# Kernel tuning notes

Hardware: AMD Instinct MI355X
Metric: run time of the kernel (lower is better)

Reference implementation:

```python
import jax, jax.numpy as jnp
import numpy as np

N_NODES = 100000
N_EDGES = 1200000
N_GRAPHS = 512
N_REL = 3
NUM_SHAPES = 16
NUM_COLORS = 16
NUM_CLASS = 10


def setup_inputs() -> dict:
    key = jax.random.key(0)
    ks = jax.random.split(key, 16)
    inp = {
        "x": jax.random.randint(ks[0], (N_NODES, 2), 0, NUM_SHAPES),
        "edge_index": jax.random.randint(ks[1], (2, N_EDGES), 0, N_NODES),
        "edge_type": jax.random.randint(ks[2], (N_EDGES,), 0, N_REL),
        "batch": jnp.sort(jax.random.randint(ks[3], (N_NODES,), 0, N_GRAPHS)),
        # parameters
        "se": jax.random.normal(ks[4], (NUM_SHAPES, 8), jnp.float32) * 0.1,
        "ce": jax.random.normal(ks[5], (NUM_COLORS, 8), jnp.float32) * 0.1,
        "pre_w": jax.random.normal(ks[6], (16, 32), jnp.float32) * 0.1,
        "pre_b": jnp.zeros((32,), jnp.float32),
        "w1": jax.random.normal(ks[7], (N_REL, 32, 64), jnp.float32) * 0.1,
        "root1": jax.random.normal(ks[8], (32, 64), jnp.float32) * 0.1,
        "b1": jnp.zeros((64,), jnp.float32),
        "w2": jax.random.normal(ks[9], (N_REL, 64, 64), jnp.float32) * 0.1,
        "root2": jax.random.normal(ks[10], (64, 64), jnp.float32) * 0.1,
        "b2": jnp.zeros((64,), jnp.float32),
        "cls_w": jax.random.normal(ks[11], (64, NUM_CLASS), jnp.float32) * 0.1,
        "cls_b": jnp.zeros((NUM_CLASS,), jnp.float32),
    }
    return inp


def _rgcn(h, src, dst, edge_type, weight, root, bias):
    # PyG RGCNConv with aggr='mean': out = x @ root + bias + sum_r mean_{edges of rel r}(x_j @ W_r)
    out = h @ root + bias
    for r in range(N_REL):
        mask = (edge_type == r)
        hr = h @ weight[r]                      # [N, out] transform-then-gather
        msg = jnp.where(mask[:, None], hr[src], 0.0)  # [E, out]
        agg = jax.ops.segment_sum(msg, dst, num_segments=N_NODES)
        cnt = jax.ops.segment_sum(mask.astype(h.dtype), dst, num_segments=N_NODES)
        out = out + agg / jnp.maximum(cnt, 1.0)[:, None]
    return out


def reference(x, edge_index, edge_type, batch, se, ce, pre_w, pre_b,
              w1, root1, b1, w2, root2, b2, cls_w, cls_b):
    h = jnp.concatenate([se[x[:, 0]], ce[x[:, 1]]], axis=1)  # [N,16]
    h = jax.nn.relu(h @ pre_w + pre_b)                        # [N,32]
    src, dst = edge_index[0], edge_index[1]
    h = jax.nn.relu(_rgcn(h, src, dst, edge_type, w1, root1, b1))  # [N,64]
    h = jax.nn.relu(_rgcn(h, src, dst, edge_type, w2, root2, b2))  # [N,64]
    # global mean pool over graph ids
    s = jax.ops.segment_sum(h, batch, num_segments=N_GRAPHS)
    c = jax.ops.segment_sum(jnp.ones((h.shape[0],), h.dtype), batch, num_segments=N_GRAPHS)
    g = s / jnp.maximum(c, 1.0)[:, None]                      # [G,64]
    return g @ cls_w + cls_b                                  # [G,num_class]
```

## Files before the change

kernel.cpp:

```cpp
#include <hip/hip_runtime.h>

#define NN 100000
#define NE 1200000
#define NG 512
#define NSEG (3 * NN)
#define NC 4
#define CHUNK 1024
#define NCHUNK ((NSEG + CHUNK - 1) / CHUNK)

typedef __bf16 bf16x8 __attribute__((ext_vector_type(8)));
typedef float f32x4 __attribute__((ext_vector_type(4)));

static constexpr size_t AGG_OFF   = 0;
static constexpr size_t AGG_BYTES = (size_t)NSEG * 32 * 4;
static constexpr size_t HIST_OFF  = AGG_OFF + AGG_BYTES;
static constexpr size_t START_OFF = HIST_OFF + (size_t)NC * NSEG * 4;
static constexpr size_t END_OFF   = START_OFF + (size_t)NSEG * 4;
static constexpr size_t COFF_OFF  = END_OFF + (size_t)NSEG * 4;
static constexpr size_t CSUM_OFF  = COFF_OFF + (size_t)NSEG * 4;
static constexpr size_t ESRC_OFF  = CSUM_OFF + 4096;
static constexpr size_t H1_OFF    = ESRC_OFF + (size_t)NE * 4;
static constexpr size_t H2_OFF    = H1_OFF + (size_t)NN * 64 * 2;
static constexpr size_t WT1H_OFF  = H2_OFF + (size_t)NN * 64 * 4;
static constexpr size_t WT1L_OFF  = WT1H_OFF + 64 * 128 * 2;
static constexpr size_t WT2H_OFF  = WT1L_OFF + 64 * 128 * 2;
static constexpr size_t WT2L_OFF  = WT2H_OFF + 64 * 256 * 2;
static constexpr size_t TAB_OFF   = WT2L_OFF + 64 * 256 * 2;
static constexpr size_t CB_OFF    = TAB_OFF + 256 * 32 * 4;
static constexpr size_t RS_OFF    = ((CB_OFF + NN + 15) / 16) * 16;

__device__ __forceinline__ void async_copy16(void* lds, const void* g) {
    __builtin_amdgcn_global_load_lds(
        (const __attribute__((address_space(1))) void*)g,
        (__attribute__((address_space(3))) void*)lds, 16, 0, 0);
}

__device__ __forceinline__ void prepw_elem(const float* root, const float* w,
                                           __bf16* wh, __bf16* wl, int cin, int t) {
    int kt = 4 * cin;
    if (t >= 64 * kt) return;
    int j = t / kt, k = t % kt;
    int sidx = k / cin, kk = k % cin;
    float v = (sidx == 0) ? root[kk * 64 + j]
                          : w[((size_t)(sidx - 1) * cin + kk) * 64 + j];
    __bf16 h = (__bf16)v;
    wh[t] = h;
    wl[t] = (__bf16)(v - (float)h);
}

#define RB_BASE 488
__global__ __launch_bounds__(256)
void k_rank_prep(const int* __restrict__ ei, const int* __restrict__ et,
                 int* __restrict__ hist4, unsigned long long* __restrict__ rs8,
                 const int* __restrict__ x, const float* __restrict__ se,
                 const float* __restrict__ ce, const float* __restrict__ pw,
                 const float* __restrict__ pb,
                 const float* __restrict__ root1, const float* __restrict__ w1,
                 const float* __restrict__ root2, const float* __restrict__ w2,
                 __bf16* __restrict__ wh1, __bf16* __restrict__ wl1,
                 __bf16* __restrict__ wh2, __bf16* __restrict__ wl2,
                 float* __restrict__ table, unsigned char* __restrict__ cb) {
    int b = blockIdx.x, t = threadIdx.x;
    if (b >= RB_BASE) {
        int e = (b - RB_BASE) * 256 + t;
        if (e >= NE) return;
        int s = ei[e];
        int d = ei[NE + e];
        int r = et[e];
        int x0 = x[2 * s], x1 = x[2 * s + 1];
        int seg = r * NN + d;
        int c = e & (NC - 1);
        unsigned int rank = (unsigned int)atomicAdd(&hist4[c * NSEG + seg], 1);
        unsigned int hi = (rank << 19) | (unsigned int)seg;
        unsigned int lo = (unsigned int)(s | ((x0 * 16 + x1) << 17));
        rs8[e] = ((unsigned long long)hi << 32) | lo;
        return;
    }
    if (b < 32) {
        prepw_elem(root1, w1, wh1, wl1, 32, b * 256 + t);
    } else if (b < 96) {
        prepw_elem(root2, w2, wh2, wl2, 64, (b - 32) * 256 + t);
    } else if (b == 96) {
        __shared__ float sW[16 * 32];
        __shared__ float sB[32];
        for (int i = t; i < 512; i += 256) sW[i] = pw[i];
        if (t < 32) sB[t] = pb[t];
        __syncthreads();
        int cmb = t, s = cmb >> 4, c = cmb & 15;
        float in[16];
#pragma unroll
        for (int k = 0; k < 8; k++) in[k] = se[s * 8 + k];
#pragma unroll
        for (int k = 0; k < 8; k++) in[8 + k] = ce[c * 8 + k];
        float acc[32];
#pragma unroll
        for (int j = 0; j < 32; j++) acc[j] = sB[j];
#pragma unroll
        for (int k = 0; k < 16; k++) {
            float hv = in[k];
#pragma unroll
            for (int j = 0; j < 32; j++) acc[j] += hv * sW[k * 32 + j];
        }
        float* o = table + (size_t)cmb * 32;
#pragma unroll
        for (int j = 0; j < 32; j += 4)
            *(float4*)(o + j) = make_float4(fmaxf(acc[j], 0.f), fmaxf(acc[j + 1], 0.f),
                                            fmaxf(acc[j + 2], 0.f), fmaxf(acc[j + 3], 0.f));
    } else {
        int n = (b - 97) * 256 + t;
        if (n < NN) cb[n] = (unsigned char)(x[2 * n] * 16 + x[2 * n + 1]);
    }
}

__global__ __launch_bounds__(256)
void k_chunksum(const int* __restrict__ hist4, int* __restrict__ csum) {
    __shared__ int s[256];
    int b = blockIdx.x, t = threadIdx.x;
    int base = b * CHUNK + t * 4;
    int sum = 0;
#pragma unroll
    for (int k = 0; k < 4; k++) {
        int i = base + k;
        if (i < NSEG) {
#pragma unroll
            for (int c = 0; c < NC; c++) sum += hist4[c * NSEG + i];
        }
    }
    s[t] = sum;
    __syncthreads();
    for (int off = 128; off > 0; off >>= 1) {
        if (t < off) s[t] += s[t + off];
        __syncthreads();
    }
    if (t == 0) csum[b] = s[0];
}

__global__ __launch_bounds__(512)
void k_chunkscan(int* __restrict__ csum) {
    __shared__ int s[512];
    int t = threadIdx.x;
    int v = (t < NCHUNK) ? csum[t] : 0;
    s[t] = v;
    __syncthreads();
    for (int off = 1; off < 512; off <<= 1) {
        int x = (t >= off) ? s[t - off] : 0;
        __syncthreads();
        s[t] += x;
        __syncthreads();
    }
    if (t < NCHUNK) csum[t] = s[t] - v;
}

__global__ __launch_bounds__(256)
void k_localscan(const int* __restrict__ hist4, const int* __restrict__ csum,
                 int* __restrict__ start, int* __restrict__ end, int* __restrict__ coff) {
    __shared__ int s[256];
    int b = blockIdx.x, t = threadIdx.x;
    int base = b * CHUNK + t * 4;
    int tot[4], cofv[4];
    int s4 = 0;
#pragma unroll
    for (int k = 0; k < 4; k++) {
        int i = base + k;
        int c0 = 0, c1 = 0, c2 = 0, c3 = 0;
        if (i < NSEG) {
            c0 = hist4[0 * NSEG + i];
            c1 = hist4[1 * NSEG + i];
            c2 = hist4[2 * NSEG + i];
            c3 = hist4[3 * NSEG + i];
        }
        tot[k] = c0 + c1 + c2 + c3;
        cofv[k] = c0 | ((c0 + c1) << 8) | ((c0 + c1 + c2) << 16);
        s4 += tot[k];
    }
    s[t] = s4;
    __syncthreads();
    for (int off = 1; off < 256; off <<= 1) {
        int x = (t >= off) ? s[t - off] : 0;
        __syncthreads();
        s[t] += x;
        __syncthreads();
    }
    int excl = s[t] - s4 + csum[b];
#pragma unroll
    for (int k = 0; k < 4; k++) {
        int i = base + k;
        if (i < NSEG) {
            start[i] = excl;
            end[i] = excl + tot[k];
            coff[i] = cofv[k];
        }
        excl += tot[k];
    }
}

__global__ __launch_bounds__(256)
void k_fill2(const unsigned long long* __restrict__ rs8,
             const int* __restrict__ start, const int* __restrict__ coff,
             int* __restrict__ esrc) {
    int e = blockIdx.x * 256 + threadIdx.x;
    if (e >= NE) return;
    unsigned long long v = rs8[e];
    unsigned int hi = (unsigned int)(v >> 32);
    int seg = (int)(hi & 0x7FFFFu);
    int rank = (int)(hi >> 19);
    int c = e & (NC - 1);
    int off = c ? ((coff[seg] >> (8 * (c - 1))) & 0xFF) : 0;
    esrc[start[seg] + off + rank] = (int)(unsigned int)v;
}

__global__ __launch_bounds__(256)
void k_gather_t(const int* __restrict__ start, const int* __restrict__ end,
                const int* __restrict__ esrc, const float* __restrict__ table,
                float* __restrict__ agg) {
    int tid = blockIdx.x * 256 + threadIdx.x;
    int seg = tid >> 3;
    int p = tid & 7;
    if (seg >= NSEG) return;
    int st = start[seg], en = end[seg];
    float4 acc = make_float4(0.f, 0.f, 0.f, 0.f);
    int i = st;
    for (; i + 4 <= en; i += 4) {
        int v0 = esrc[i], v1 = esrc[i + 1], v2 = esrc[i + 2], v3 = esrc[i + 3];
        float4 a = *(const float4*)(table + ((v0 >> 17) & 0xFF) * 32 + p * 4);
        float4 b = *(const float4*)(table + ((v1 >> 17) & 0xFF) * 32 + p * 4);
        float4 c = *(const float4*)(table + ((v2 >> 17) & 0xFF) * 32 + p * 4);
        float4 d = *(const float4*)(table + ((v3 >> 17) & 0xFF) * 32 + p * 4);
        acc.x += (a.x + b.x) + (c.x + d.x);
        acc.y += (a.y + b.y) + (c.y + d.y);
        acc.z += (a.z + b.z) + (c.z + d.z);
        acc.w += (a.w + b.w) + (c.w + d.w);
    }
    for (; i < en; i++) {
        int v = esrc[i];
        float4 a = *(const float4*)(table + ((v >> 17) & 0xFF) * 32 + p * 4);
        acc.x += a.x; acc.y += a.y; acc.z += a.z; acc.w += a.w;
    }
    int c = en - st;
    float inv = 1.f / (float)(c > 1 ? c : 1);
    acc.x *= inv; acc.y *= inv; acc.z *= inv; acc.w *= inv;
    *(float4*)(agg + (size_t)seg * 32 + p * 4) = acc;
}

__global__ __launch_bounds__(256)
void k_gather64(const int* __restrict__ start, const int* __restrict__ end,
                const int* __restrict__ esrc, const __bf16* __restrict__ h,
                __bf16* __restrict__ agg) {
    int tid = blockIdx.x * 256 + threadIdx.x;
    int seg = tid >> 3;
    int p = tid & 7;
    if (seg >= NSEG) return;
    int st = start[seg], en = end[seg];
    float acc[8];
#pragma unroll
    for (int j = 0; j < 8; j++) acc[j] = 0.f;
    int i = st;
    for (; i + 4 <= en; i += 4) {
        int s0 = esrc[i] & 0x1FFFF, s1 = esrc[i + 1] & 0x1FFFF;
        int s2 = esrc[i + 2] & 0x1FFFF, s3 = esrc[i + 3] & 0x1FFFF;
        bf16x8 v0 = *(const bf16x8*)(h + (size_t)s0 * 64 + p * 8);
        bf16x8 v1 = *(const bf16x8*)(h + (size_t)s1 * 64 + p * 8);
        bf16x8 v2 = *(const bf16x8*)(h + (size_t)s2 * 64 + p * 8);
        bf16x8 v3 = *(const bf16x8*)(h + (size_t)s3 * 64 + p * 8);
#pragma unroll
        for (int j = 0; j < 8; j++)
            acc[j] += ((float)v0[j] + (float)v1[j]) + ((float)v2[j] + (float)v3[j]);
    }
    for (; i < en; i++) {
        int s = esrc[i] & 0x1FFFF;
        bf16x8 v = *(const bf16x8*)(h + (size_t)s * 64 + p * 8);
#pragma unroll
        for (int j = 0; j < 8; j++) acc[j] += (float)v[j];
    }
    int c = en - st;
    float inv = 1.f / (float)(c > 1 ? c : 1);
    bf16x8 o;
#pragma unroll
    for (int j = 0; j < 8; j++) o[j] = (__bf16)(acc[j] * inv);
    *(bf16x8*)(agg + (size_t)seg * 64 + p * 8) = o;
}

__device__ __forceinline__ void split8(float4 a0, float4 a1, bf16x8& hi, bf16x8& lo) {
    float v[8] = {a0.x, a0.y, a0.z, a0.w, a1.x, a1.y, a1.z, a1.w};
#pragma unroll
    for (int i = 0; i < 8; i++) {
        __bf16 h = (__bf16)v[i];
        hi[i] = h;
        lo[i] = (__bf16)(v[i] - (float)h);
    }
}

__global__ __launch_bounds__(256, 1)
void k_combine_l1(const float* __restrict__ table, const unsigned char* __restrict__ cb,
                  const float* __restrict__ agg,
                  const __bf16* __restrict__ wh, const __bf16* __restrict__ wl,
                  const float* __restrict__ bias, __bf16* __restrict__ h_out) {
    constexpr int KT = 128;
    __shared__ float sIN[64 * 64];
    __shared__ __bf16 sWH[64 * 64];
    __shared__ __bf16 sWL[64 * 64];

    const int tid = threadIdx.x;
    const int wave = tid >> 6;
    const int lane = tid & 63;
    const int cA = lane & 15;
    const int kg = lane >> 4;
    const int n0 = blockIdx.x * 64;

    f32x4 acc[4];
#pragma unroll
    for (int nb = 0; nb < 4; nb++) {
        float bv = bias[nb * 16 + cA];
        acc[nb][0] = bv; acc[nb][1] = bv; acc[nb][2] = bv; acc[nb][3] = bv;
    }

    for (int c = 0; c < 2; c++) {
        if (c) __syncthreads();
#pragma unroll
        for (int i = 0; i < 4; i++) {
            int F = tid + i * 256;
            int row = F >> 4, j = F & 15;
            int jor = j ^ (row & 7);
            int n = n0 + row; if (n > NN - 1) n = NN - 1;
            int sidx = 2 * c + (jor >> 3);
            int jj = jor & 7;
            const float* src = (sidx == 0)
                ? table + (size_t)cb[n] * 32 + jj * 4
                : agg + ((size_t)(sidx - 1) * NN + n) * 32 + jj * 4;
            async_copy16(sIN + (size_t)F * 4, src);
        }
#pragma unroll
        for (int i = 0; i < 2; i++) {
            int F = tid + i * 256;
            int col = F >> 3, s = F & 7;
            int sor = s ^ (col & 7);
            async_copy16(sWH + (size_t)F * 8, wh + (size_t)col * KT + c * 64 + sor * 8);
            async_copy16(sWL + (size_t)F * 8, wl + (size_t)col * KT + c * 64 + sor * 8);
        }
        __syncthreads();
#pragma unroll
        for (int ks = 0; ks < 2; ks++) {
            const int rowL = wave * 16 + cA;
            const int jA = ks * 8 + kg * 2;
            float4 a0 = ((const float4*)sIN)[rowL * 16 + (jA ^ (rowL & 7))];
            float4 a1 = ((const float4*)sIN)[rowL * 16 + ((jA + 1) ^ (rowL & 7))];
            bf16x8 ah, al;
            split8(a0, a1, ah, al);
            const int k8 = ks * 4 + kg;
#pragma unroll
            for (int nb = 0; nb < 4; nb++) {
                const int col = nb * 16 + cA;
                const int bs = col * 8 + (k8 ^ (col & 7));
                bf16x8 bh = ((const bf16x8*)sWH)[bs];
                bf16x8 bl = ((const bf16x8*)sWL)[bs];
                acc[nb] = __builtin_amdgcn_mfma_f32_16x16x32_bf16(ah, bh, acc[nb], 0, 0, 0);
                acc[nb] = __builtin_amdgcn_mfma_f32_16x16x32_bf16(al, bh, acc[nb], 0, 0, 0);
                acc[nb] = __builtin_amdgcn_mfma_f32_16x16x32_bf16(ah, bl, acc[nb], 0, 0, 0);
                acc[nb] = __builtin_amdgcn_mfma_f32_16x16x32_bf16(al, bl, acc[nb], 0, 0, 0);
            }
        }
    }
#pragma unroll
    for (int nb = 0; nb < 4; nb++) {
#pragma unroll
        for (int r = 0; r < 4; r++) {
            int n = n0 + wave * 16 + kg * 4 + r;
            if (n < NN)
                h_out[(size_t)n * 64 + nb * 16 + cA] = (__bf16)fmaxf(acc[nb][r], 0.f);
        }
    }
}

__global__ __launch_bounds__(256, 1)
void k_combine_l2(const __bf16* __restrict__ h1b, const __bf16* __restrict__ aggb,
                  const __bf16* __restrict__ wh, const __bf16* __restrict__ wl,
                  const float* __restrict__ bias, float* __restrict__ h_out) {
    constexpr int KT = 256;
    __shared__ __bf16 sINb[64 * 64];
    __shared__ __bf16 sWH[64 * 64];
    __shared__ __bf16 sWL[64 * 64];

    const int tid = threadIdx.x;
    const int wave = tid >> 6;
    const int lane = tid & 63;
    const int cA = lane & 15;
    const int kg = lane >> 4;
    const int n0 = blockIdx.x * 64;

    f32x4 acc[4];
#pragma unroll
    for (int nb = 0; nb < 4; nb++) {
        float bv = bias[nb * 16 + cA];
        acc[nb][0] = bv; acc[nb][1] = bv; acc[nb][2] = bv; acc[nb][3] = bv;
    }

    for (int c = 0; c < 4; c++) {
        if (c) __syncthreads();
#pragma unroll
        for (int i = 0; i < 2; i++) {
            int F = tid + i * 256;
            int row = F >> 3, j = F & 7;
            int jor = j ^ (row & 7);
            int n = n0 + row; if (n > NN - 1) n = NN - 1;
            const __bf16* src = (c == 0)
                ? h1b + (size_t)n * 64 + jor * 8
                : aggb + ((size_t)(c - 1) * NN + n) * 64 + jor * 8;
            async_copy16(sINb + (size_t)F * 8, src);
        }
#pragma unroll
        for (int i = 0; i < 2; i++) {
            int F = tid + i * 256;
            int col = F >> 3, s = F & 7;
            int sor = s ^ (col & 7);
            async_copy16(sWH + (size_t)F * 8, wh + (size_t)col * KT + c * 64 + sor * 8);
            async_copy16(sWL + (size_t)F * 8, wl + (size_t)col * KT + c * 64 + sor * 8);
        }
        __syncthreads();
#pragma unroll
        for (int ks = 0; ks < 2; ks++) {
            const int rowL = wave * 16 + cA;
            const int s8 = ks * 4 + kg;
            bf16x8 ah = ((const bf16x8*)sINb)[rowL * 8 + (s8 ^ (rowL & 7))];
#pragma unroll
            for (int nb = 0; nb < 4; nb++) {
                const int col = nb * 16 + cA;
                const int bs = col * 8 + (s8 ^ (col & 7));
                bf16x8 bh = ((const bf16x8*)sWH)[bs];
                bf16x8 bl = ((const bf16x8*)sWL)[bs];
                acc[nb] = __builtin_amdgcn_mfma_f32_16x16x32_bf16(ah, bh, acc[nb], 0, 0, 0);
                acc[nb] = __builtin_amdgcn_mfma_f32_16x16x32_bf16(ah, bl, acc[nb], 0, 0, 0);
            }
        }
    }
#pragma unroll
    for (int nb = 0; nb < 4; nb++) {
#pragma unroll
        for (int r = 0; r < 4; r++) {
            int n = n0 + wave * 16 + kg * 4 + r;
            if (n < NN)
                h_out[(size_t)n * 64 + nb * 16 + cA] = fmaxf(acc[nb][r], 0.f);
        }
    }
}

__global__ __launch_bounds__(256)
void k_pool_final(const float* __restrict__ h, const int* __restrict__ batch,
                  const float* __restrict__ cw, const float* __restrict__ cbias,
                  float* __restrict__ out) {
    int g = blockIdx.x;
    auto lb = [&](int v) {
        int lo = 0, hi = NN;
        while (lo < hi) {
            int m = (lo + hi) >> 1;
            if (batch[m] < v) lo = m + 1; else hi = m;
        }
        return lo;
    };
    int st = lb(g), en = lb(g + 1);
    int col = threadIdx.x & 63, chunk = threadIdx.x >> 6;
    float acc = 0.f;
    for (int n = st + chunk; n < en; n += 4) acc += h[(size_t)n * 64 + col];
    __shared__ float s[256];
    __shared__ float mean[64];
    s[threadIdx.x] = acc;
    __syncthreads();
    if (chunk == 0) {
        float tot = s[col] + s[64 + col] + s[128 + col] + s[192 + col];
        int c = en - st;
        mean[col] = tot / (float)(c > 1 ? c : 1);
    }
    __syncthreads();
    if (threadIdx.x < 10) {
        int j = threadIdx.x;
        float o = cbias[j];
#pragma unroll
        for (int k = 0; k < 64; k++) o += mean[k] * cw[k * 10 + j];
        out[g * 10 + j] = o;
    }
}

extern "C" void kernel_launch(void* const* d_in, const int* in_sizes, int n_in,
                              void* d_out, int out_size, void* d_ws, size_t ws_size,
                              hipStream_t stream) {
    const int* x      = (const int*)d_in[0];
    const int* ei     = (const int*)d_in[1];
    const int* et     = (const int*)d_in[2];
    const int* batch  = (const int*)d_in[3];
    const float* se   = (const float*)d_in[4];
    const float* ce   = (const float*)d_in[5];
    const float* pw   = (const float*)d_in[6];
    const float* pb   = (const float*)d_in[7];
    const float* w1   = (const float*)d_in[8];
    const float* root1= (const float*)d_in[9];
    const float* b1   = (const float*)d_in[10];
    const float* w2   = (const float*)d_in[11];
    const float* root2= (const float*)d_in[12];
    const float* b2   = (const float*)d_in[13];
    const float* cw   = (const float*)d_in[14];
    const float* cbias= (const float*)d_in[15];
    float* out = (float*)d_out;

    char* ws = (char*)d_ws;
    float*  agg1 = (float*)(ws + AGG_OFF);
    __bf16* aggb = (__bf16*)(ws + AGG_OFF);
    int*   hist4 = (int*)(ws + HIST_OFF);
    int*   start = (int*)(ws + START_OFF);
    int*   end   = (int*)(ws + END_OFF);
    int*   coff  = (int*)(ws + COFF_OFF);
    int*   csum  = (int*)(ws + CSUM_OFF);
    int*   esrc  = (int*)(ws + ESRC_OFF);
    __bf16* h1b  = (__bf16*)(ws + H1_OFF);
    float* h2    = (float*)(ws + H2_OFF);
    __bf16* wt1h = (__bf16*)(ws + WT1H_OFF);
    __bf16* wt1l = (__bf16*)(ws + WT1L_OFF);
    __bf16* wt2h = (__bf16*)(ws + WT2H_OFF);
    __bf16* wt2l = (__bf16*)(ws + WT2L_OFF);
    float* table = (float*)(ws + TAB_OFF);
    unsigned char* cbarr = (unsigned char*)(ws + CB_OFF);
    unsigned long long* rs8 = (unsigned long long*)(ws + RS_OFF);

    (void)hipMemsetAsync(hist4, 0, (size_t)NC * NSEG * 4, stream);

    int rank_blocks = RB_BASE + (NE + 255) / 256;
    k_rank_prep<<<rank_blocks, 256, 0, stream>>>(ei, et, hist4, rs8,
                                                 x, se, ce, pw, pb, root1, w1, root2, w2,
                                                 wt1h, wt1l, wt2h, wt2l, table, cbarr);

    k_chunksum<<<NCHUNK, 256, 0, stream>>>(hist4, csum);
    k_chunkscan<<<1, 512, 0, stream>>>(csum);
    k_localscan<<<NCHUNK, 256, 0, stream>>>(hist4, csum, start, end, coff);
    k_fill2<<<(NE + 255) / 256, 256, 0, stream>>>(rs8, start, coff, esrc);

    k_gather_t<<<(NSEG * 8 + 255) / 256, 256, 0, stream>>>(start, end, esrc, table, agg1);
    k_combine_l1<<<(NN + 63) / 64, 256, 0, stream>>>(table, cbarr, agg1,
                                                     wt1h, wt1l, b1, h1b);
    k_gather64<<<(NSEG * 8 + 255) / 256, 256, 0, stream>>>(start, end, esrc, h1b, aggb);
    k_combine_l2<<<(NN + 63) / 64, 256, 0, stream>>>(h1b, aggb,
                                                     wt2h, wt2l, b2, h2);

    k_pool_final<<<NG, 256, 0, stream>>>(h2, batch, cw, cbias, out);
}
```

Baseline: 197.4 us.

## Precompute layer-1 transformed combo tables and fuse gather with combine

Each node's layer-1 input depends only on its 256 possible (shape,color) combos, so the code now precomputes the combo table multiplied by root1 (plus bias) and by each relation weight, giving four 256x64 tables. A single kernel then gathers the transformed rows per relation, mean-normalises, adds the root term, applies ReLU and writes h1 in bf16. This removes the float agg1 intermediate and the MFMA combine_l1 kernel. In exchange, gathered rows are twice as wide (64 floats instead of 32) and one thread loops over all three relations serially.

```diff
diff --git a/kernel.cpp b/kernel.cpp
--- a/kernel.cpp
+++ b/kernel.cpp
@@ -12,7 +12,7 @@
 typedef float f32x4 __attribute__((ext_vector_type(4)));
 
 static constexpr size_t AGG_OFF   = 0;
-static constexpr size_t AGG_BYTES = (size_t)NSEG * 32 * 4;
+static constexpr size_t AGG_BYTES = (size_t)NSEG * 64 * 2;
 static constexpr size_t HIST_OFF  = AGG_OFF + AGG_BYTES;
 static constexpr size_t START_OFF = HIST_OFF + (size_t)NC * NSEG * 4;
 static constexpr size_t END_OFF   = START_OFF + (size_t)NSEG * 4;
@@ -21,12 +21,10 @@
 static constexpr size_t ESRC_OFF  = CSUM_OFF + 4096;
 static constexpr size_t H1_OFF    = ESRC_OFF + (size_t)NE * 4;
 static constexpr size_t H2_OFF    = H1_OFF + (size_t)NN * 64 * 2;
-static constexpr size_t WT1H_OFF  = H2_OFF + (size_t)NN * 64 * 4;
-static constexpr size_t WT1L_OFF  = WT1H_OFF + 64 * 128 * 2;
-static constexpr size_t WT2H_OFF  = WT1L_OFF + 64 * 128 * 2;
+static constexpr size_t WT2H_OFF  = H2_OFF + (size_t)NN * 64 * 4;
 static constexpr size_t WT2L_OFF  = WT2H_OFF + 64 * 256 * 2;
-static constexpr size_t TAB_OFF   = WT2L_OFF + 64 * 256 * 2;
-static constexpr size_t CB_OFF    = TAB_OFF + 256 * 32 * 4;
+static constexpr size_t TW_OFF    = WT2L_OFF + 64 * 256 * 2;
+static constexpr size_t CB_OFF    = TW_OFF + 4 * 256 * 64 * 4;
 static constexpr size_t RS_OFF    = ((CB_OFF + NN + 15) / 16) * 16;
 
 __device__ __forceinline__ void async_copy16(void* lds, const void* g) {
@@ -48,7 +46,28 @@
     wl[t] = (__bf16)(v - (float)h);
 }
 
-#define RB_BASE 488
+__device__ __forceinline__ void combo_row(int cmb, const float* se, const float* ce,
+                                          const float* sW, const float* sB, float* outr) {
+    int s = cmb >> 4, c = cmb & 15;
+    float in[16];
+#pragma unroll
+    for (int k = 0; k < 8; k++) in[k] = se[s * 8 + k];
+#pragma unroll
+    for (int k = 0; k < 8; k++) in[8 + k] = ce[c * 8 + k];
+    float acc[32];
+#pragma unroll
+    for (int j = 0; j < 32; j++) acc[j] = sB[j];
+#pragma unroll
+    for (int k = 0; k < 16; k++) {
+        float hv = in[k];
+#pragma unroll
+        for (int j = 0; j < 32; j++) acc[j] += hv * sW[k * 32 + j];
+    }
+#pragma unroll
+    for (int j = 0; j < 32; j++) outr[j] = fmaxf(acc[j], 0.f);
+}
+
+#define RB_BASE 471
 __global__ __launch_bounds__(256)
 void k_rank_prep(const int* __restrict__ ei, const int* __restrict__ et,
                  int* __restrict__ hist4, unsigned long long* __restrict__ rs8,
@@ -56,10 +75,10 @@
                  const float* __restrict__ ce, const float* __restrict__ pw,
                  const float* __restrict__ pb,
                  const float* __restrict__ root1, const float* __restrict__ w1,
+                 const float* __restrict__ b1,
                  const float* __restrict__ root2, const float* __restrict__ w2,
-                 __bf16* __restrict__ wh1, __bf16* __restrict__ wl1,
                  __bf16* __restrict__ wh2, __bf16* __restrict__ wl2,
-                 float* __restrict__ table, unsigned char* __restrict__ cb) {
+                 float* __restrict__ tw, unsigned char* __restrict__ cb) {
     int b = blockIdx.x, t = threadIdx.x;
     if (b >= RB_BASE) {
         int e = (b - RB_BASE) * 256 + t;
@@ -76,38 +95,40 @@
         rs8[e] = ((unsigned long long)hi << 32) | lo;
         return;
     }
-    if (b < 32) {
-        prepw_elem(root1, w1, wh1, wl1, 32, b * 256 + t);
-    } else if (b < 96) {
-        prepw_elem(root2, w2, wh2, wl2, 64, (b - 32) * 256 + t);
-    } else if (b == 96) {
+    if (b < 64) {
+        prepw_elem(root2, w2, wh2, wl2, 64, b * 256 + t);
+    } else if (b < 80) {
         __shared__ float sW[16 * 32];
         __shared__ float sB[32];
+        __shared__ float sTab[256 * 33];
         for (int i = t; i < 512; i += 256) sW[i] = pw[i];
         if (t < 32) sB[t] = pb[t];
         __syncthreads();
-        int cmb = t, s = cmb >> 4, c = cmb & 15;
-        float in[16];
-#pragma unroll
-        for (int k = 0; k < 8; k++) in[k] = se[s * 8 + k];
-#pragma unroll
-        for (int k = 0; k < 8; k++) in[8 + k] = ce[c * 8 + k];
-        float acc[32];
-#pragma unroll
-        for (int j = 0; j < 32; j++) acc[j] = sB[j];
-#pragma unroll
-        for (int k = 0; k < 16; k++) {
-            float hv = in[k];
-#pragma unroll
-            for (int j = 0; j < 32; j++) acc[j] += hv * sW[k * 32 + j];
-        }
-        float* o = table + (size_t)cmb * 32;
-#pragma unroll
-        for (int j = 0; j < 32; j += 4)
-            *(float4*)(o + j) = make_float4(fmaxf(acc[j], 0.f), fmaxf(acc[j + 1], 0.f),
-                                            fmaxf(acc[j + 2], 0.f), fmaxf(acc[j + 3], 0.f));
+        {
+            float row[32];
+            combo_row(t, se, ce, sW, sB, row);
+#pragma unroll
+            for (int j = 0; j < 32; j++) sTab[t * 33 + j] = row[j];
+        }
+        __syncthreads();
+        int ti = (b - 64) >> 2;
+        int row = ((b - 64) & 3) * 64 + (t >> 2);
+        int c0 = (t & 3) * 16;
+        const float* Wsrc = (ti == 0) ? root1 : (w1 + (size_t)(ti - 1) * 32 * 64);
+        float acc[16];
+#pragma unroll
+        for (int j = 0; j < 16; j++) acc[j] = (ti == 0) ? b1[c0 + j] : 0.f;
+        for (int k = 0; k < 32; k++) {
+            float hv = sTab[row * 33 + k];
+#pragma unroll
+            for (int j = 0; j < 16; j++) acc[j] += hv * Wsrc[k * 64 + c0 + j];
+        }
+        float* o = tw + (size_t)ti * 256 * 64 + (size_t)row * 64 + c0;
+#pragma unroll
+        for (int j = 0; j < 16; j += 4)
+            *(float4*)(o + j) = make_float4(acc[j], acc[j + 1], acc[j + 2], acc[j + 3]);
     } else {
-        int n = (b - 97) * 256 + t;
+        int n = (b - 80) * 256 + t;
         if (n < NN) cb[n] = (unsigned char)(x[2 * n] * 16 + x[2 * n + 1]);
     }
 }
@@ -210,36 +231,42 @@
 }
 
 __global__ __launch_bounds__(256)
-void k_gather_t(const int* __restrict__ start, const int* __restrict__ end,
-                const int* __restrict__ esrc, const float* __restrict__ table,
-                float* __restrict__ agg) {
+void k_l1(const int* __restrict__ start, const int* __restrict__ end,
+          const int* __restrict__ esrc, const unsigned char* __restrict__ cb,
+          const float* __restrict__ tw, __bf16* __restrict__ h1b) {
     int tid = blockIdx.x * 256 + threadIdx.x;
-    int seg = tid >> 3;
+    int n = tid >> 3;
     int p = tid & 7;
-    if (seg >= NSEG) return;
-    int st = start[seg], en = end[seg];
-    float4 acc = make_float4(0.f, 0.f, 0.f, 0.f);
-    int i = st;
-    for (; i + 4 <= en; i += 4) {
-        int v0 = esrc[i], v1 = esrc[i + 1], v2 = esrc[i + 2], v3 = esrc[i + 3];
-        float4 a = *(const float4*)(table + ((v0 >> 17) & 0xFF) * 32 + p * 4);
-        float4 b = *(const float4*)(table + ((v1 >> 17) & 0xFF) * 32 + p * 4);
-        float4 c = *(const float4*)(table + ((v2 >> 17) & 0xFF) * 32 + p * 4);
-        float4 d = *(const float4*)(table + ((v3 >> 17) & 0xFF) * 32 + p * 4);
-        acc.x += (a.x + b.x) + (c.x + d.x);
-        acc.y += (a.y + b.y) + (c.y + d.y);
-        acc.z += (a.z + b.z) + (c.z + d.z);
-        acc.w += (a.w + b.w) + (c.w + d.w);
-    }
-    for (; i < en; i++) {
-        int v = esrc[i];
-        float4 a = *(const float4*)(table + ((v >> 17) & 0xFF) * 32 + p * 4);
-        acc.x += a.x; acc.y += a.y; acc.z += a.z; acc.w += a.w;
-    }
-    int c = en - st;
-    float inv = 1.f / (float)(c > 1 ? c : 1);
-    acc.x *= inv; acc.y *= inv; acc.z *= inv; acc.w *= inv;
-    *(float4*)(agg + (size_t)seg * 32 + p * 4) = acc;
+    if (n >= NN) return;
+    const float* tr = tw + (size_t)cb[n] * 64 + p * 8;
+    float4 a0 = *(const float4*)tr;
+    float4 a1 = *(const float4*)(tr + 4);
+#pragma unroll
+    for (int r = 0; r < 3; r++) {
+        const float* tb = tw + (size_t)(r + 1) * 256 * 64 + p * 8;
+        int seg = r * NN + n;
+        int st = start[seg], en = end[seg];
+        float4 r0 = make_float4(0.f, 0.f, 0.f, 0.f);
+        float4 r1 = make_float4(0.f, 0.f, 0.f, 0.f);
+        for (int i = st; i < en; i++) {
+            int cmb = (esrc[i] >> 17) & 0xFF;
+            const float* row = tb + (size_t)cmb * 64;
+            float4 v0 = *(const float4*)row;
+            float4 v1 = *(const float4*)(row + 4);
+            r0.x += v0.x; r0.y += v0.y; r0.z += v0.z; r0.w += v0.w;
+            r1.x += v1.x; r1.y += v1.y; r1.z += v1.z; r1.w += v1.w;
+        }
+        int c = en - st;
+        float inv = 1.f / (float)(c > 1 ? c : 1);
+        a0.x += r0.x * inv; a0.y += r0.y * inv; a0.z += r0.z * inv; a0.w += r0.w * inv;
+        a1.x += r1.x * inv; a1.y += r1.y * inv; a1.z += r1.z * inv; a1.w += r1.w * inv;
+    }
+    bf16x8 o;
+    o[0] = (__bf16)fmaxf(a0.x, 0.f); o[1] = (__bf16)fmaxf(a0.y, 0.f);
+    o[2] = (__bf16)fmaxf(a0.z, 0.f); o[3] = (__bf16)fmaxf(a0.w, 0.f);
+    o[4] = (__bf16)fmaxf(a1.x, 0.f); o[5] = (__bf16)fmaxf(a1.y, 0.f);
+    o[6] = (__bf16)fmaxf(a1.z, 0.f); o[7] = (__bf16)fmaxf(a1.w, 0.f);
+    *(bf16x8*)(h1b + (size_t)n * 64 + p * 8) = o;
 }
 
 __global__ __launch_bounds__(256)
@@ -278,97 +305,6 @@
 #pragma unroll
     for (int j = 0; j < 8; j++) o[j] = (__bf16)(acc[j] * inv);
     *(bf16x8*)(agg + (size_t)seg * 64 + p * 8) = o;
-}
-
-__device__ __forceinline__ void split8(float4 a0, float4 a1, bf16x8& hi, bf16x8& lo) {
-    float v[8] = {a0.x, a0.y, a0.z, a0.w, a1.x, a1.y, a1.z, a1.w};
-#pragma unroll
-    for (int i = 0; i < 8; i++) {
-        __bf16 h = (__bf16)v[i];
-        hi[i] = h;
-        lo[i] = (__bf16)(v[i] - (float)h);
-    }
-}
-
-__global__ __launch_bounds__(256, 1)
-void k_combine_l1(const float* __restrict__ table, const unsigned char* __restrict__ cb,
-                  const float* __restrict__ agg,
-                  const __bf16* __restrict__ wh, const __bf16* __restrict__ wl,
-                  const float* __restrict__ bias, __bf16* __restrict__ h_out) {
-    constexpr int KT = 128;
-    __shared__ float sIN[64 * 64];
-    __shared__ __bf16 sWH[64 * 64];
-    __shared__ __bf16 sWL[64 * 64];
-
-    const int tid = threadIdx.x;
-    const int wave = tid >> 6;
-    const int lane = tid & 63;
-    const int cA = lane & 15;
-    const int kg = lane >> 4;
-    const int n0 = blockIdx.x * 64;
-
-    f32x4 acc[4];
-#pragma unroll
-    for (int nb = 0; nb < 4; nb++) {
-        float bv = bias[nb * 16 + cA];
-        acc[nb][0] = bv; acc[nb][1] = bv; acc[nb][2] = bv; acc[nb][3] = bv;
-    }
-
-    for (int c = 0; c < 2; c++) {
-        if (c) __syncthreads();
-#pragma unroll
-        for (int i = 0; i < 4; i++) {
-            int F = tid + i * 256;
-            int row = F >> 4, j = F & 15;
-            int jor = j ^ (row & 7);
-            int n = n0 + row; if (n > NN - 1) n = NN - 1;
-            int sidx = 2 * c + (jor >> 3);
-            int jj = jor & 7;
-            const float* src = (sidx == 0)
-                ? table + (size_t)cb[n] * 32 + jj * 4
-                : agg + ((size_t)(sidx - 1) * NN + n) * 32 + jj * 4;
-            async_copy16(sIN + (size_t)F * 4, src);
-        }
-#pragma unroll
-        for (int i = 0; i < 2; i++) {
-            int F = tid + i * 256;
-            int col = F >> 3, s = F & 7;
-            int sor = s ^ (col & 7);
-            async_copy16(sWH + (size_t)F * 8, wh + (size_t)col * KT + c * 64 + sor * 8);
-            async_copy16(sWL + (size_t)F * 8, wl + (size_t)col * KT + c * 64 + sor * 8);
-        }
-        __syncthreads();
-#pragma unroll
-        for (int ks = 0; ks < 2; ks++) {
-            const int rowL = wave * 16 + cA;
-            const int jA = ks * 8 + kg * 2;
-            float4 a0 = ((const float4*)sIN)[rowL * 16 + (jA ^ (rowL & 7))];
-            float4 a1 = ((const float4*)sIN)[rowL * 16 + ((jA + 1) ^ (rowL & 7))];
-            bf16x8 ah, al;
-            split8(a0, a1, ah, al);
-            const int k8 = ks * 4 + kg;
-#pragma unroll
-            for (int nb = 0; nb < 4; nb++) {
-                const int col = nb * 16 + cA;
-                const int bs = col * 8 + (k8 ^ (col & 7));
-                bf16x8 bh = ((const bf16x8*)sWH)[bs];
-                bf16x8 bl = ((const bf16x8*)sWL)[bs];
-                acc[nb] = __builtin_amdgcn_mfma_f32_16x16x32_bf16(ah, bh, acc[nb], 0, 0, 0);
-                acc[nb] = __builtin_amdgcn_mfma_f32_16x16x32_bf16(al, bh, acc[nb], 0, 0, 0);
-                acc[nb] = __builtin_amdgcn_mfma_f32_16x16x32_bf16(ah, bl, acc[nb], 0, 0, 0);
-                acc[nb] = __builtin_amdgcn_mfma_f32_16x16x32_bf16(al, bl, acc[nb], 0, 0, 0);
-            }
-        }
-    }
-#pragma unroll
-    for (int nb = 0; nb < 4; nb++) {
-#pragma unroll
-        for (int r = 0; r < 4; r++) {
-            int n = n0 + wave * 16 + kg * 4 + r;
-            if (n < NN)
-                h_out[(size_t)n * 64 + nb * 16 + cA] = (__bf16)fmaxf(acc[nb][r], 0.f);
-        }
-    }
 }
 
 __global__ __launch_bounds__(256, 1)
@@ -501,7 +437,6 @@
     float* out = (float*)d_out;
 
     char* ws = (char*)d_ws;
-    float*  agg1 = (float*)(ws + AGG_OFF);
     __bf16* aggb = (__bf16*)(ws + AGG_OFF);
     int*   hist4 = (int*)(ws + HIST_OFF);
     int*   start = (int*)(ws + START_OFF);
@@ -511,11 +446,9 @@
     int*   esrc  = (int*)(ws + ESRC_OFF);
     __bf16* h1b  = (__bf16*)(ws + H1_OFF);
     float* h2    = (float*)(ws + H2_OFF);
-    __bf16* wt1h = (__bf16*)(ws + WT1H_OFF);
-    __bf16* wt1l = (__bf16*)(ws + WT1L_OFF);
     __bf16* wt2h = (__bf16*)(ws + WT2H_OFF);
     __bf16* wt2l = (__bf16*)(ws + WT2L_OFF);
-    float* table = (float*)(ws + TAB_OFF);
+    float* tw    = (float*)(ws + TW_OFF);
     unsigned char* cbarr = (unsigned char*)(ws + CB_OFF);
     unsigned long long* rs8 = (unsigned long long*)(ws + RS_OFF);
 
@@ -523,17 +456,17 @@
 
     int rank_blocks = RB_BASE + (NE + 255) / 256;
     k_rank_prep<<<rank_blocks, 256, 0, stream>>>(ei, et, hist4, rs8,
-                                                 x, se, ce, pw, pb, root1, w1, root2, w2,
-                                                 wt1h, wt1l, wt2h, wt2l, table, cbarr);
+                                                 x, se, ce, pw, pb,
+                                                 root1, w1, b1, root2, w2,
+                                                 wt2h, wt2l, tw, cbarr);
 
     k_chunksum<<<NCHUNK, 256, 0, stream>>>(hist4, csum);
     k_chunkscan<<<1, 512, 0, stream>>>(csum);
     k_localscan<<<NCHUNK, 256, 0, stream>>>(hist4, csum, start, end, coff);
     k_fill2<<<(NE + 255) / 256, 256, 0, stream>>>(rs8, start, coff, esrc);
 
-    k_gather_t<<<(NSEG * 8 + 255) / 256, 256, 0, stream>>>(start, end, esrc, table, agg1);
-    k_combine_l1<<<(NN + 63) / 64, 256, 0, stream>>>(table, cbarr, agg1,
-                                                     wt1h, wt1l, b1, h1b);
+    k_l1<<<(NN * 8 + 255) / 256, 256, 0, stream>>>(start, end, esrc, cbarr, tw, h1b);
+
     k_gather64<<<(NSEG * 8 + 255) / 256, 256, 0, stream>>>(start, end, esrc, h1b, aggb);
     k_combine_l2<<<(NN + 63) / 64, 256, 0, stream>>>(h1b, aggb,
                                                      wt2h, wt2l, b2, h2);
```

After: 193.7 us. No clear change (-1.9%).
